# Kernel optimization log

Measured on AMD Instinct MI355X. Metric: run time of the kernel, lower is better.

## Reference

```python
import jax, jax.numpy as jnp
import numpy as np

ACT_BW = 8
PAR_BW = 4
EPS = 1e-8

def fake_quant(t, bw):
    # symmetric per-tensor fake quantization with dynamic absmax observer
    qmax = float(2 ** (bw - 1) - 1)
    scale = jnp.maximum(jnp.max(jnp.abs(t)) / qmax, EPS)
    q = jnp.clip(jnp.round(t / scale), -qmax, qmax) * scale
    # straight-through estimator (matches torch fake-quant backward)
    return t + jax.lax.stop_gradient(q - t)

def setup_inputs() -> dict:
    key = jax.random.key(0)
    k1, k2, k3 = jax.random.split(key, 3)
    tokens, d_in, d_out = 4096, 4096, 4096
    x = jax.random.normal(k1, (tokens, d_in), dtype=jnp.float32)
    # kaiming-uniform-ish init scale
    bound_w = 1.0 / np.sqrt(d_in)
    weight = jax.random.uniform(k2, (d_out, d_in), dtype=jnp.float32, minval=-bound_w, maxval=bound_w)
    b = jax.random.uniform(k3, (d_out,), dtype=jnp.float32, minval=-bound_w, maxval=bound_w)
    return {"x": x, "weight": weight, "b": b}

def reference(x, weight, b):
    # 1) requantize input activations (act_bitwidth)
    xq = fake_quant(x, ACT_BW)
    # 2) quantize weight (par_bitwidth), transpose [out,in] -> [in,out]
    wq = fake_quant(weight, PAR_BW).T
    # 3) quantize bias (act_bitwidth)
    bq = fake_quant(b, ACT_BW)
    # 4) AddMM: bias + x @ w^T, then requantize the output (multiplier's quantizer)
    out = bq + jnp.matmul(xq, wq)  # [tokens, out_features]
    return fake_quant(out, ACT_BW)
```

## Files before the change

kernel.cpp:

```cpp
#include <hip/hip_runtime.h>

#define NELEM (4096 * 4096)
#define KDIM 4096
#define NDIM 4096
#define DOUT 4096
#define EPSQ 1e-8f

typedef __attribute__((ext_vector_type(4))) int i32x4;

typedef __attribute__((address_space(3))) void lds_void;
typedef const __attribute__((address_space(1))) void gbl_void;

__device__ __forceinline__ void load_lds16(const void* g, void* l) {
    __builtin_amdgcn_global_load_lds((gbl_void*)g, (lds_void*)l, 16, 0, 0);
}

__device__ __forceinline__ float wave_max64(float v) {
#pragma unroll
    for (int off = 32; off > 0; off >>= 1)
        v = fmaxf(v, __shfl_down(v, off));
    return v;
}

__global__ void zero_ws(unsigned* __restrict__ amax) {
    if (threadIdx.x < 4) amax[threadIdx.x] = 0u;
}

__global__ __launch_bounds__(256) void absmax_xwb(
    const float4* __restrict__ x, const float4* __restrict__ w,
    const float* __restrict__ b, unsigned* __restrict__ amax)
{
    const int n4 = NELEM / 4;
    float mx = 0.f, mw = 0.f;
    for (int i = blockIdx.x * 256 + threadIdx.x; i < n4; i += gridDim.x * 256) {
        float4 a = x[i];
        mx = fmaxf(mx, fmaxf(fmaxf(fabsf(a.x), fabsf(a.y)), fmaxf(fabsf(a.z), fabsf(a.w))));
        float4 c = w[i];
        mw = fmaxf(mw, fmaxf(fmaxf(fabsf(c.x), fabsf(c.y)), fmaxf(fabsf(c.z), fabsf(c.w))));
    }
    float mb = 0.f;
    if (blockIdx.x == 0)
        for (int i = threadIdx.x; i < DOUT; i += 256) mb = fmaxf(mb, fabsf(b[i]));

    mx = wave_max64(mx); mw = wave_max64(mw); mb = wave_max64(mb);
    __shared__ float red[3][4];
    const int wave = threadIdx.x >> 6, lane = threadIdx.x & 63;
    if (lane == 0) { red[0][wave] = mx; red[1][wave] = mw; red[2][wave] = mb; }
    __syncthreads();
    if (threadIdx.x == 0) {
        float r0 = fmaxf(fmaxf(red[0][0], red[0][1]), fmaxf(red[0][2], red[0][3]));
        float r1 = fmaxf(fmaxf(red[1][0], red[1][1]), fmaxf(red[1][2], red[1][3]));
        atomicMax(&amax[0], __float_as_uint(r0));
        atomicMax(&amax[1], __float_as_uint(r1));
        if (blockIdx.x == 0) {
            float r2 = fmaxf(fmaxf(red[2][0], red[2][1]), fmaxf(red[2][2], red[2][3]));
            atomicMax(&amax[2], __float_as_uint(r2));
        }
    }
}

__device__ __forceinline__ int pack4(float4 a, float s, float qmax) {
    int b0 = (int)fminf(fmaxf(rintf(a.x / s), -qmax), qmax);
    int b1 = (int)fminf(fmaxf(rintf(a.y / s), -qmax), qmax);
    int b2 = (int)fminf(fmaxf(rintf(a.z / s), -qmax), qmax);
    int b3 = (int)fminf(fmaxf(rintf(a.w / s), -qmax), qmax);
    return (b0 & 0xff) | ((b1 & 0xff) << 8) | ((b2 & 0xff) << 16) | (b3 << 24);
}

__global__ __launch_bounds__(256) void quant_xwb(
    const float4* __restrict__ x, const float4* __restrict__ w,
    const float* __restrict__ b, const unsigned* __restrict__ amax,
    int4* __restrict__ qx, int4* __restrict__ qw, float* __restrict__ bq)
{
    const float sx = fmaxf(__uint_as_float(amax[0]) / 127.0f, EPSQ);
    const float sw = fmaxf(__uint_as_float(amax[1]) / 7.0f, EPSQ);
    const int n16 = NELEM / 16;
    for (int i = blockIdx.x * 256 + threadIdx.x; i < n16; i += gridDim.x * 256) {
        int4 r;
        r.x = pack4(x[i * 4 + 0], sx, 127.f);
        r.y = pack4(x[i * 4 + 1], sx, 127.f);
        r.z = pack4(x[i * 4 + 2], sx, 127.f);
        r.w = pack4(x[i * 4 + 3], sx, 127.f);
        qx[i] = r;
        int4 p;
        p.x = pack4(w[i * 4 + 0], sw, 7.f);
        p.y = pack4(w[i * 4 + 1], sw, 7.f);
        p.z = pack4(w[i * 4 + 2], sw, 7.f);
        p.w = pack4(w[i * 4 + 3], sw, 7.f);
        qw[i] = p;
    }
    if (blockIdx.x == 0) {
        const float sb = fmaxf(__uint_as_float(amax[2]) / 127.0f, EPSQ);
        for (int i = threadIdx.x; i < DOUT; i += 256) {
            float q = fminf(fmaxf(rintf(b[i] / sb), -127.f), 127.f);
            bq[i] = q * sb;
        }
    }
}

__global__ __launch_bounds__(256, 2) void gemm_i8(
    const char* __restrict__ qx,
    const char* __restrict__ qw,
    const float* __restrict__ bq,
    const unsigned* __restrict__ amax,
    float* __restrict__ out,
    unsigned* __restrict__ amax_out)
{
    constexpr int K = KDIM, N = NDIM, BK = 64;
    __shared__ char smemA[128 * BK];
    __shared__ char smemB[128 * BK];
    __shared__ float red[4];

    const int tid = threadIdx.x;
    const int wave = tid >> 6;
    const int lane = tid & 63;
    const int bm = blockIdx.y, bn = blockIdx.x;

    const int wm = (wave & 1) * 64;
    const int wn = (wave >> 1) * 64;

    i32x4 acc[4][4] = {};

    const int srow = wave * 16 + (lane >> 2);
    const int scol = (lane & 3) * 16;
    const char* aP0 = qx + (long)(bm * 128 + srow) * K + scol;
    const char* aP1 = aP0 + 64 * K;
    const char* bP0 = qw + (long)(bn * 128 + srow) * K + scol;
    const char* bP1 = bP0 + 64 * K;
    char* aL0 = smemA + wave * 1024;
    char* aL1 = aL0 + 4096;
    char* bL0 = smemB + wave * 1024;
    char* bL1 = bL0 + 4096;

    const int frow = lane & 15;
    const int fk = (lane >> 4) * 16;

    for (int k0 = 0; k0 < K; k0 += BK) {
        __syncthreads();
        load_lds16(aP0 + k0, aL0);
        load_lds16(aP1 + k0, aL1);
        load_lds16(bP0 + k0, bL0);
        load_lds16(bP1 + k0, bL1);
        __syncthreads();

        i32x4 af[4], bf[4];
#pragma unroll
        for (int i = 0; i < 4; ++i)
            af[i] = *(const i32x4*)(smemA + (wm + i * 16 + frow) * BK + fk);
#pragma unroll
        for (int j = 0; j < 4; ++j)
            bf[j] = *(const i32x4*)(smemB + (wn + j * 16 + frow) * BK + fk);
#pragma unroll
        for (int i = 0; i < 4; ++i)
#pragma unroll
            for (int j = 0; j < 4; ++j)
                acc[i][j] = __builtin_amdgcn_mfma_i32_16x16x64_i8(af[i], bf[j], acc[i][j], 0, 0, 0);
    }

    const float sx = fmaxf(__uint_as_float(amax[0]) / 127.0f, EPSQ);
    const float sw = fmaxf(__uint_as_float(amax[1]) / 7.0f, EPSQ);
    const float s = sx * sw;
    const int col = lane & 15;
    const int rbase = (lane >> 4) * 4;
    float am = 0.f;
    float bqv[4];
#pragma unroll
    for (int j = 0; j < 4; ++j) bqv[j] = bq[bn * 128 + wn + j * 16 + col];

#pragma unroll
    for (int i = 0; i < 4; ++i) {
#pragma unroll
        for (int r = 0; r < 4; ++r) {
            const int m = bm * 128 + wm + i * 16 + rbase + r;
            float* orow = out + (long)m * N + bn * 128 + wn + col;
#pragma unroll
            for (int j = 0; j < 4; ++j) {
                float o = fmaf(s, (float)acc[i][j][r], bqv[j]);
                am = fmaxf(am, fabsf(o));
                orow[j * 16] = o;
            }
        }
    }
    am = wave_max64(am);
    if (lane == 0) red[wave] = am;
    __syncthreads();
    if (tid == 0)
        atomicMax(amax_out, __float_as_uint(fmaxf(fmaxf(red[0], red[1]), fmaxf(red[2], red[3]))));
}

__global__ __launch_bounds__(256) void final_quant(
    float4* __restrict__ out, const unsigned* __restrict__ amax)
{
    const float so = fmaxf(__uint_as_float(amax[3]) / 127.0f, EPSQ);
    const int n4 = NELEM / 4;
    for (int i = blockIdx.x * 256 + threadIdx.x; i < n4; i += gridDim.x * 256) {
        float4 v = out[i];
        v.x = fminf(fmaxf(rintf(v.x / so), -127.f), 127.f) * so;
        v.y = fminf(fmaxf(rintf(v.y / so), -127.f), 127.f) * so;
        v.z = fminf(fmaxf(rintf(v.z / so), -127.f), 127.f) * so;
        v.w = fminf(fmaxf(rintf(v.w / so), -127.f), 127.f) * so;
        out[i] = v;
    }
}

extern "C" void kernel_launch(void* const* d_in, const int* in_sizes, int n_in,
                              void* d_out, int out_size, void* d_ws, size_t ws_size,
                              hipStream_t stream) {
    const float* x = (const float*)d_in[0];
    const float* w = (const float*)d_in[1];
    const float* b = (const float*)d_in[2];
    float* out = (float*)d_out;

    char* ws = (char*)d_ws;
    unsigned* amax = (unsigned*)ws;
    float* bq = (float*)(ws + 256);
    char* qx = (char*)(ws + 32768);
    char* qw = (char*)(ws + 32768 + (size_t)NELEM);

    hipLaunchKernelGGL(zero_ws, dim3(1), dim3(64), 0, stream, amax);
    hipLaunchKernelGGL(absmax_xwb, dim3(2048), dim3(256), 0, stream,
                       (const float4*)x, (const float4*)w, b, amax);
    hipLaunchKernelGGL(quant_xwb, dim3(2048), dim3(256), 0, stream,
                       (const float4*)x, (const float4*)w, b, amax,
                       (int4*)qx, (int4*)qw, bq);
    hipLaunchKernelGGL(gemm_i8, dim3(32, 32), dim3(256), 0, stream,
                       qx, qw, bq, amax, out, amax + 3);
    hipLaunchKernelGGL(final_quant, dim3(2048), dim3(256), 0, stream,
                       (float4*)out, amax);
}
```

Baseline: 317.7 us.

## Fuse all stages into one persistent kernel with software grid barriers

Replaces the five launches with a single persistent kernel of 512 blocks. Software grid barriers sit between the absmax, quantize, GEMM and output-quantize phases. Each block computes two 128x128 output tiles and keeps their accumulators in registers until the global output absmax is known. It then writes the quantized output once, which removes the separate full-size output read-modify-write pass and the extra launches. The trade-offs are higher register pressure, and the barriers require all 512 blocks to be co-resident, otherwise the kernel deadlocks.

```diff
diff --git a/kernel.cpp b/kernel.cpp
--- a/kernel.cpp
+++ b/kernel.cpp
@@ -3,11 +3,10 @@
 #define NELEM (4096 * 4096)
 #define KDIM 4096
 #define NDIM 4096
-#define DOUT 4096
 #define EPSQ 1e-8f
+#define NBLK 512
 
 typedef __attribute__((ext_vector_type(4))) int i32x4;
-
 typedef __attribute__((address_space(3))) void lds_void;
 typedef const __attribute__((address_space(1))) void gbl_void;
 
@@ -22,41 +21,34 @@
     return v;
 }
 
-__global__ void zero_ws(unsigned* __restrict__ amax) {
-    if (threadIdx.x < 4) amax[threadIdx.x] = 0u;
-}
-
-__global__ __launch_bounds__(256) void absmax_xwb(
-    const float4* __restrict__ x, const float4* __restrict__ w,
-    const float* __restrict__ b, unsigned* __restrict__ amax)
-{
-    const int n4 = NELEM / 4;
-    float mx = 0.f, mw = 0.f;
-    for (int i = blockIdx.x * 256 + threadIdx.x; i < n4; i += gridDim.x * 256) {
-        float4 a = x[i];
-        mx = fmaxf(mx, fmaxf(fmaxf(fabsf(a.x), fabsf(a.y)), fmaxf(fabsf(a.z), fabsf(a.w))));
-        float4 c = w[i];
-        mw = fmaxf(mw, fmaxf(fmaxf(fabsf(c.x), fabsf(c.y)), fmaxf(fabsf(c.z), fabsf(c.w))));
-    }
-    float mb = 0.f;
-    if (blockIdx.x == 0)
-        for (int i = threadIdx.x; i < DOUT; i += 256) mb = fmaxf(mb, fabsf(b[i]));
-
-    mx = wave_max64(mx); mw = wave_max64(mw); mb = wave_max64(mb);
-    __shared__ float red[3][4];
-    const int wave = threadIdx.x >> 6, lane = threadIdx.x & 63;
-    if (lane == 0) { red[0][wave] = mx; red[1][wave] = mw; red[2][wave] = mb; }
-    __syncthreads();
-    if (threadIdx.x == 0) {
-        float r0 = fmaxf(fmaxf(red[0][0], red[0][1]), fmaxf(red[0][2], red[0][3]));
-        float r1 = fmaxf(fmaxf(red[1][0], red[1][1]), fmaxf(red[1][2], red[1][3]));
-        atomicMax(&amax[0], __float_as_uint(r0));
-        atomicMax(&amax[1], __float_as_uint(r1));
-        if (blockIdx.x == 0) {
-            float r2 = fmaxf(fmaxf(red[2][0], red[2][1]), fmaxf(red[2][2], red[2][3]));
-            atomicMax(&amax[2], __float_as_uint(r2));
-        }
-    }
+__device__ __forceinline__ float block_max(float v, float* redf) {
+    v = wave_max64(v);
+    __syncthreads();
+    if ((threadIdx.x & 63) == 0) redf[threadIdx.x >> 6] = v;
+    __syncthreads();
+    return fmaxf(fmaxf(redf[0], redf[1]), fmaxf(redf[2], redf[3]));
+}
+
+__device__ __forceinline__ void grid_barrier(unsigned* flags, unsigned* go, unsigned gen) {
+    __syncthreads();
+    if (blockIdx.x == 0) {
+        if (threadIdx.x == 0)
+            __hip_atomic_store(&flags[0], gen, __ATOMIC_RELEASE, __HIP_MEMORY_SCOPE_AGENT);
+        while (__hip_atomic_load(&flags[threadIdx.x], __ATOMIC_ACQUIRE, __HIP_MEMORY_SCOPE_AGENT) != gen)
+            __builtin_amdgcn_s_sleep(1);
+        while (__hip_atomic_load(&flags[threadIdx.x + 256], __ATOMIC_ACQUIRE, __HIP_MEMORY_SCOPE_AGENT) != gen)
+            __builtin_amdgcn_s_sleep(1);
+        __syncthreads();
+        if (threadIdx.x == 0)
+            __hip_atomic_store(go, gen, __ATOMIC_RELEASE, __HIP_MEMORY_SCOPE_AGENT);
+    } else {
+        if (threadIdx.x == 0) {
+            __hip_atomic_store(&flags[blockIdx.x], gen, __ATOMIC_RELEASE, __HIP_MEMORY_SCOPE_AGENT);
+            while (__hip_atomic_load(go, __ATOMIC_ACQUIRE, __HIP_MEMORY_SCOPE_AGENT) != gen)
+                __builtin_amdgcn_s_sleep(1);
+        }
+    }
+    __syncthreads();
 }
 
 __device__ __forceinline__ int pack4(float4 a, float s, float qmax) {
@@ -67,140 +59,181 @@
     return (b0 & 0xff) | ((b1 & 0xff) << 8) | ((b2 & 0xff) << 16) | (b3 << 24);
 }
 
-__global__ __launch_bounds__(256) void quant_xwb(
-    const float4* __restrict__ x, const float4* __restrict__ w,
-    const float* __restrict__ b, const unsigned* __restrict__ amax,
-    int4* __restrict__ qx, int4* __restrict__ qw, float* __restrict__ bq)
+__global__ __launch_bounds__(256, 2) void fused_all(
+    const float* __restrict__ x,
+    const float* __restrict__ w,
+    const float* __restrict__ b,
+    float* __restrict__ out,
+    char* __restrict__ ws)
 {
-    const float sx = fmaxf(__uint_as_float(amax[0]) / 127.0f, EPSQ);
-    const float sw = fmaxf(__uint_as_float(amax[1]) / 7.0f, EPSQ);
-    const int n16 = NELEM / 16;
-    for (int i = blockIdx.x * 256 + threadIdx.x; i < n16; i += gridDim.x * 256) {
-        int4 r;
-        r.x = pack4(x[i * 4 + 0], sx, 127.f);
-        r.y = pack4(x[i * 4 + 1], sx, 127.f);
-        r.z = pack4(x[i * 4 + 2], sx, 127.f);
-        r.w = pack4(x[i * 4 + 3], sx, 127.f);
-        qx[i] = r;
-        int4 p;
-        p.x = pack4(w[i * 4 + 0], sw, 7.f);
-        p.y = pack4(w[i * 4 + 1], sw, 7.f);
-        p.z = pack4(w[i * 4 + 2], sw, 7.f);
-        p.w = pack4(w[i * 4 + 3], sw, 7.f);
-        qw[i] = p;
-    }
-    if (blockIdx.x == 0) {
-        const float sb = fmaxf(__uint_as_float(amax[2]) / 127.0f, EPSQ);
-        for (int i = threadIdx.x; i < DOUT; i += 256) {
-            float q = fminf(fmaxf(rintf(b[i] / sb), -127.f), 127.f);
-            bq[i] = q * sb;
-        }
-    }
-}
-
-__global__ __launch_bounds__(256, 2) void gemm_i8(
-    const char* __restrict__ qx,
-    const char* __restrict__ qw,
-    const float* __restrict__ bq,
-    const unsigned* __restrict__ amax,
-    float* __restrict__ out,
-    unsigned* __restrict__ amax_out)
-{
-    constexpr int K = KDIM, N = NDIM, BK = 64;
-    __shared__ char smemA[128 * BK];
-    __shared__ char smemB[128 * BK];
-    __shared__ float red[4];
-
-    const int tid = threadIdx.x;
-    const int wave = tid >> 6;
-    const int lane = tid & 63;
-    const int bm = blockIdx.y, bn = blockIdx.x;
-
+    unsigned* flags  = (unsigned*)ws;
+    unsigned* go     = (unsigned*)(ws + 2048);
+    float* pmax_x = (float*)(ws + 4096);
+    float* pmax_w = (float*)(ws + 6144);
+    float* pmax_b = (float*)(ws + 8192);
+    float* omax   = (float*)(ws + 8448);
+    float* bq     = (float*)(ws + 12288);
+    char*  qx     = ws + 32768;
+    char*  qw     = qx + (size_t)NELEM;
+
+    const int bid = blockIdx.x, tid = threadIdx.x;
+    __shared__ float redf[4];
+    __shared__ char smA[128 * 64];
+    __shared__ char smB[128 * 64];
+
+    {
+        const float4* x4 = (const float4*)x;
+        const float4* w4 = (const float4*)w;
+        float mx = 0.f, mw = 0.f;
+        for (int i = bid * 256 + tid; i < NELEM / 4; i += NBLK * 256) {
+            float4 a = x4[i];
+            mx = fmaxf(mx, fmaxf(fmaxf(fabsf(a.x), fabsf(a.y)), fmaxf(fabsf(a.z), fabsf(a.w))));
+            float4 c = w4[i];
+            mw = fmaxf(mw, fmaxf(fmaxf(fabsf(c.x), fabsf(c.y)), fmaxf(fabsf(c.z), fabsf(c.w))));
+        }
+        float mb = 0.f;
+        if (bid == 0)
+            for (int i = tid; i < NDIM; i += 256) mb = fmaxf(mb, fabsf(b[i]));
+        mx = block_max(mx, redf);
+        mw = block_max(mw, redf);
+        mb = block_max(mb, redf);
+        if (tid == 0) {
+            pmax_x[bid] = mx;
+            pmax_w[bid] = mw;
+            if (bid == 0) pmax_b[0] = mb;
+        }
+    }
+    grid_barrier(flags, go, 1u);
+
+    float vx = fmaxf(pmax_x[tid], pmax_x[tid + 256]);
+    float vw = fmaxf(pmax_w[tid], pmax_w[tid + 256]);
+    vx = block_max(vx, redf);
+    vw = block_max(vw, redf);
+    const float sx = fmaxf(vx / 127.0f, EPSQ);
+    const float sw = fmaxf(vw / 7.0f, EPSQ);
+    const float s = sx * sw;
+
+    {
+        const float4* x4 = (const float4*)x;
+        const float4* w4 = (const float4*)w;
+        int4* qx4 = (int4*)qx;
+        int4* qw4 = (int4*)qw;
+        for (int i = bid * 256 + tid; i < NELEM / 16; i += NBLK * 256) {
+            int4 r;
+            r.x = pack4(x4[i * 4 + 0], sx, 127.f);
+            r.y = pack4(x4[i * 4 + 1], sx, 127.f);
+            r.z = pack4(x4[i * 4 + 2], sx, 127.f);
+            r.w = pack4(x4[i * 4 + 3], sx, 127.f);
+            qx4[i] = r;
+            int4 p;
+            p.x = pack4(w4[i * 4 + 0], sw, 7.f);
+            p.y = pack4(w4[i * 4 + 1], sw, 7.f);
+            p.z = pack4(w4[i * 4 + 2], sw, 7.f);
+            p.w = pack4(w4[i * 4 + 3], sw, 7.f);
+            qw4[i] = p;
+        }
+        if (bid == 0) {
+            const float sb = fmaxf(pmax_b[0] / 127.0f, EPSQ);
+            for (int i = tid; i < NDIM; i += 256) {
+                float q = fminf(fmaxf(rintf(b[i] / sb), -127.f), 127.f);
+                bq[i] = q * sb;
+            }
+        }
+    }
+    grid_barrier(flags, go, 2u);
+
+    const int wave = tid >> 6, lane = tid & 63;
     const int wm = (wave & 1) * 64;
     const int wn = (wave >> 1) * 64;
-
-    i32x4 acc[4][4] = {};
-
     const int srow = wave * 16 + (lane >> 2);
     const int scol = (lane & 3) * 16;
-    const char* aP0 = qx + (long)(bm * 128 + srow) * K + scol;
-    const char* aP1 = aP0 + 64 * K;
-    const char* bP0 = qw + (long)(bn * 128 + srow) * K + scol;
-    const char* bP1 = bP0 + 64 * K;
-    char* aL0 = smemA + wave * 1024;
+    char* aL0 = smA + wave * 1024;
     char* aL1 = aL0 + 4096;
-    char* bL0 = smemB + wave * 1024;
+    char* bL0 = smB + wave * 1024;
     char* bL1 = bL0 + 4096;
-
     const int frow = lane & 15;
     const int fk = (lane >> 4) * 16;
 
-    for (int k0 = 0; k0 < K; k0 += BK) {
-        __syncthreads();
-        load_lds16(aP0 + k0, aL0);
-        load_lds16(aP1 + k0, aL1);
-        load_lds16(bP0 + k0, bL0);
-        load_lds16(bP1 + k0, bL1);
-        __syncthreads();
-
-        i32x4 af[4], bf[4];
-#pragma unroll
-        for (int i = 0; i < 4; ++i)
-            af[i] = *(const i32x4*)(smemA + (wm + i * 16 + frow) * BK + fk);
-#pragma unroll
-        for (int j = 0; j < 4; ++j)
-            bf[j] = *(const i32x4*)(smemB + (wn + j * 16 + frow) * BK + fk);
-#pragma unroll
-        for (int i = 0; i < 4; ++i)
+    i32x4 acc[2][4][4] = {};
+    int bmv[2], bnv[2];
+
+#pragma unroll
+    for (int t = 0; t < 2; ++t) {
+        const int tile = bid * 2 + t;
+        const int bm = tile >> 5, bn = tile & 31;
+        bmv[t] = bm; bnv[t] = bn;
+        const char* aP0 = qx + (long)(bm * 128 + srow) * KDIM + scol;
+        const char* aP1 = aP0 + 64 * KDIM;
+        const char* bP0 = qw + (long)(bn * 128 + srow) * KDIM + scol;
+        const char* bP1 = bP0 + 64 * KDIM;
+
+        for (int k0 = 0; k0 < KDIM; k0 += 64) {
+            __syncthreads();
+            load_lds16(aP0 + k0, aL0);
+            load_lds16(aP1 + k0, aL1);
+            load_lds16(bP0 + k0, bL0);
+            load_lds16(bP1 + k0, bL1);
+            __syncthreads();
+
+            i32x4 af[4], bf[4];
+#pragma unroll
+            for (int i = 0; i < 4; ++i)
+                af[i] = *(const i32x4*)(smA + (wm + i * 16 + frow) * 64 + fk);
 #pragma unroll
             for (int j = 0; j < 4; ++j)
-                acc[i][j] = __builtin_amdgcn_mfma_i32_16x16x64_i8(af[i], bf[j], acc[i][j], 0, 0, 0);
-    }
-
-    const float sx = fmaxf(__uint_as_float(amax[0]) / 127.0f, EPSQ);
-    const float sw = fmaxf(__uint_as_float(amax[1]) / 7.0f, EPSQ);
-    const float s = sx * sw;
+                bf[j] = *(const i32x4*)(smB + (wn + j * 16 + frow) * 64 + fk);
+#pragma unroll
+            for (int i = 0; i < 4; ++i)
+#pragma unroll
+                for (int j = 0; j < 4; ++j)
+                    acc[t][i][j] = __builtin_amdgcn_mfma_i32_16x16x64_i8(af[i], bf[j], acc[t][i][j], 0, 0, 0);
+        }
+    }
+
     const int col = lane & 15;
     const int rbase = (lane >> 4) * 4;
+    float bqv[2][4];
+#pragma unroll
+    for (int t = 0; t < 2; ++t)
+#pragma unroll
+        for (int j = 0; j < 4; ++j)
+            bqv[t][j] = bq[bnv[t] * 128 + wn + j * 16 + col];
+
     float am = 0.f;
-    float bqv[4];
-#pragma unroll
-    for (int j = 0; j < 4; ++j) bqv[j] = bq[bn * 128 + wn + j * 16 + col];
-
-#pragma unroll
-    for (int i = 0; i < 4; ++i) {
-#pragma unroll
-        for (int r = 0; r < 4; ++r) {
-            const int m = bm * 128 + wm + i * 16 + rbase + r;
-            float* orow = out + (long)m * N + bn * 128 + wn + col;
-#pragma unroll
-            for (int j = 0; j < 4; ++j) {
-                float o = fmaf(s, (float)acc[i][j][r], bqv[j]);
-                am = fmaxf(am, fabsf(o));
-                orow[j * 16] = o;
+#pragma unroll
+    for (int t = 0; t < 2; ++t)
+#pragma unroll
+        for (int i = 0; i < 4; ++i)
+#pragma unroll
+            for (int r = 0; r < 4; ++r)
+#pragma unroll
+                for (int j = 0; j < 4; ++j) {
+                    float o = fmaf(s, (float)acc[t][i][j][r], bqv[t][j]);
+                    am = fmaxf(am, fabsf(o));
+                }
+    am = block_max(am, redf);
+    if (tid == 0) omax[bid] = am;
+    grid_barrier(flags, go, 3u);
+
+    float vo = fmaxf(omax[tid], omax[tid + 256]);
+    vo = block_max(vo, redf);
+    const float so = fmaxf(vo / 127.0f, EPSQ);
+
+#pragma unroll
+    for (int t = 0; t < 2; ++t)
+#pragma unroll
+        for (int i = 0; i < 4; ++i)
+#pragma unroll
+            for (int r = 0; r < 4; ++r) {
+                const int m = bmv[t] * 128 + wm + i * 16 + rbase + r;
+                float* orow = out + (long)m * NDIM + bnv[t] * 128 + wn + col;
+#pragma unroll
+                for (int j = 0; j < 4; ++j) {
+                    float o = fmaf(s, (float)acc[t][i][j][r], bqv[t][j]);
+                    float q = fminf(fmaxf(rintf(o / so), -127.f), 127.f) * so;
+                    orow[j * 16] = q;
+                }
             }
-        }
-    }
-    am = wave_max64(am);
-    if (lane == 0) red[wave] = am;
-    __syncthreads();
-    if (tid == 0)
-        atomicMax(amax_out, __float_as_uint(fmaxf(fmaxf(red[0], red[1]), fmaxf(red[2], red[3]))));
-}
-
-__global__ __launch_bounds__(256) void final_quant(
-    float4* __restrict__ out, const unsigned* __restrict__ amax)
-{
-    const float so = fmaxf(__uint_as_float(amax[3]) / 127.0f, EPSQ);
-    const int n4 = NELEM / 4;
-    for (int i = blockIdx.x * 256 + threadIdx.x; i < n4; i += gridDim.x * 256) {
-        float4 v = out[i];
-        v.x = fminf(fmaxf(rintf(v.x / so), -127.f), 127.f) * so;
-        v.y = fminf(fmaxf(rintf(v.y / so), -127.f), 127.f) * so;
-        v.z = fminf(fmaxf(rintf(v.z / so), -127.f), 127.f) * so;
-        v.w = fminf(fmaxf(rintf(v.w / so), -127.f), 127.f) * so;
-        out[i] = v;
-    }
 }
 
 extern "C" void kernel_launch(void* const* d_in, const int* in_sizes, int n_in,
@@ -210,21 +243,7 @@
     const float* w = (const float*)d_in[1];
     const float* b = (const float*)d_in[2];
     float* out = (float*)d_out;
-
     char* ws = (char*)d_ws;
-    unsigned* amax = (unsigned*)ws;
-    float* bq = (float*)(ws + 256);
-    char* qx = (char*)(ws + 32768);
-    char* qw = (char*)(ws + 32768 + (size_t)NELEM);
-
-    hipLaunchKernelGGL(zero_ws, dim3(1), dim3(64), 0, stream, amax);
-    hipLaunchKernelGGL(absmax_xwb, dim3(2048), dim3(256), 0, stream,
-                       (const float4*)x, (const float4*)w, b, amax);
-    hipLaunchKernelGGL(quant_xwb, dim3(2048), dim3(256), 0, stream,
-                       (const float4*)x, (const float4*)w, b, amax,
-                       (int4*)qx, (int4*)qw, bq);
-    hipLaunchKernelGGL(gemm_i8, dim3(32, 32), dim3(256), 0, stream,
-                       qx, qw, bq, amax, out, amax + 3);
-    hipLaunchKernelGGL(final_quant, dim3(2048), dim3(256), 0, stream,
-                       (float4*)out, amax);
-}
+
+    hipLaunchKernelGGL(fused_all, dim3(NBLK), dim3(256), 0, stream, x, w, b, out, ws);
+}
```

Measured after the change: 409.3 us. 1.29x slower.
